# Kernel optimization log

Hardware: AMD Instinct MI355X
Metric: run time of the kernel (lower is better)

## Reference

```python
import jax, jax.numpy as jnp
import numpy as np

N = 50000      # nodes
E = 500000     # edges
F = 128        # hidden_dim
NRBF = 20
CUTOFF = 5.0


def setup_inputs() -> dict:
    key = jax.random.key(0)
    ks = jax.random.split(key, 12)
    s = jax.random.normal(ks[0], (N, F), dtype=jnp.float32)
    v = jax.random.normal(ks[1], (N, 3, F), dtype=jnp.float32)
    pos = jax.random.normal(ks[2], (N, 3), dtype=jnp.float32)
    src = jax.random.randint(ks[3], (E,), 0, N)
    # avoid self-loops so rij never degenerates to exactly zero
    off = jax.random.randint(ks[4], (E,), 1, N)
    dst = (src + off) % N
    edge_index = jnp.stack([src, dst]).astype(jnp.int64)
    in_dim = 2 * F + NRBF
    sc = 0.02
    W1 = jax.random.normal(ks[5], (in_dim, 2 * F), dtype=jnp.float32) * sc
    b1 = jnp.zeros((2 * F,), dtype=jnp.float32)
    W2 = jax.random.normal(ks[6], (2 * F, 2 * F), dtype=jnp.float32) * sc
    b2 = jnp.zeros((2 * F,), dtype=jnp.float32)
    Ws = jax.random.normal(ks[7], (2 * F, F), dtype=jnp.float32) * sc
    bs = jnp.zeros((F,), dtype=jnp.float32)
    Wv = jax.random.normal(ks[8], (2 * F, F), dtype=jnp.float32) * sc
    bv = jnp.zeros((F,), dtype=jnp.float32)
    centers = jnp.linspace(0.0, CUTOFF, NRBF).astype(jnp.float32)
    delta = centers[1] - centers[0]
    widths = jnp.full((NRBF,), delta, dtype=jnp.float32)
    return {"s": s, "v": v, "pos": pos, "edge_index": edge_index,
            "W1": W1, "b1": b1, "W2": W2, "b2": b2,
            "Ws": Ws, "bs": bs, "Wv": Wv, "bv": bv,
            "centers": centers, "widths": widths}


def reference(s, v, pos, edge_index, W1, b1, W2, b2, Ws, bs, Wv, bv, centers, widths):
    src, dst = edge_index[0], edge_index[1]
    rij = pos[dst] - pos[src]                          # [E,3]
    dist = jnp.linalg.norm(rij, axis=-1, keepdims=True)  # [E,1]
    rbf = jnp.exp(-((dist - centers) / (widths + 1e-8)) ** 2)  # [E,NRBF]
    h = jnp.concatenate([s[src], s[dst], rbf], axis=-1)  # [E, 2F+NRBF]
    h = jax.nn.silu(h @ W1 + b1)
    h = jax.nn.silu(h @ W2 + b2)                         # [E, 2F]
    ds_edge = h @ Ws + bs                                # [E, F]
    dv_mag = h @ Wv + bv                                 # [E, F]
    safe = jnp.where(dist > 0, dist, 1.0)
    inv_dist = jnp.where(dist > 0, 1.0 / safe, 0.0)
    directions = rij * inv_dist                          # [E,3]
    dv_edge = directions[:, :, None] * dv_mag[:, None, :]  # [E,3,F]
    num_nodes = s.shape[0]
    ds = jax.ops.segment_sum(ds_edge, dst, num_segments=num_nodes)   # [N,F]
    dv = jax.ops.segment_sum(dv_edge, dst, num_segments=num_nodes)   # [N,3,F]
    return s + ds, v + dv
```

## Files before the change

kernel.cpp:

```cpp
#include <hip/hip_runtime.h>
#include <math.h>

#define FDIM   128
#define TWOF   256
#define NRBF_  20
#define INDIM  276
#define K1PAD  288
#define XS     296
#define HS     264
#define EOS    264
#define TE     64

typedef __bf16 bf16x8 __attribute__((ext_vector_type(8)));
typedef __bf16 bf16x4 __attribute__((ext_vector_type(4)));
typedef float  f32x4  __attribute__((ext_vector_type(4)));

__device__ inline float blo(unsigned p){ return __uint_as_float(p << 16); }
__device__ inline float bhi(unsigned p){ return __uint_as_float(p & 0xffff0000u); }


__global__ void sniff_idx(const int* __restrict__ ei, int nsample, int* __restrict__ flag) {
    __shared__ int any;
    if (threadIdx.x == 0) any = 0;
    __syncthreads();
    int nz = 0;
    for (int i = threadIdx.x; i < nsample; i += blockDim.x)
        nz |= (ei[2 * i + 1] != 0);
    if (nz) atomicOr(&any, 1);
    __syncthreads();
    if (threadIdx.x == 0) *flag = any;
}

__global__ void init_out(const float4* __restrict__ s4, const float4* __restrict__ v4,
                         float4* __restrict__ out4, int nf4, int total4) {
    for (int i = blockIdx.x * blockDim.x + threadIdx.x; i < total4;
         i += gridDim.x * blockDim.x)
        out4[i] = (i < nf4) ? s4[i] : v4[i - nf4];
}

__global__ void prep_weights(const float* __restrict__ W1, const float* __restrict__ W2,
                             const float* __restrict__ Ws, const float* __restrict__ Wv,
                             __bf16* __restrict__ W1t, __bf16* __restrict__ W2t,
                             __bf16* __restrict__ W3t) {
    int id = blockIdx.x * 256 + threadIdx.x;
    const int n1 = 256 * K1PAD;
    if (id < n1) {
        int n = id / K1PAD, k = id - n * K1PAD;
        W1t[id] = (k < INDIM) ? (__bf16)W1[k * TWOF + n] : (__bf16)0.f;
    } else if (id < n1 + 65536) {
        int j = id - n1; int n = j >> 8, k = j & 255;
        W2t[j] = (__bf16)W2[k * TWOF + n];
    } else if (id < n1 + 131072) {
        int j = id - n1 - 65536; int n = j >> 8, k = j & 255;
        W3t[j] = (n < FDIM) ? (__bf16)Ws[k * FDIM + n]
                            : (__bf16)Wv[k * FDIM + (n - FDIM)];
    }
}


__global__ void zero_hist(int* __restrict__ hist, int N) {
    int i = blockIdx.x * 256 + threadIdx.x;
    if (i < N) hist[i] = 0;
}

__global__ void hist_k(const int* __restrict__ ei, const int* __restrict__ flag,
                       int* __restrict__ hist, int E) {
    int e = blockIdx.x * 256 + threadIdx.x;
    if (e >= E) return;
    int dst = (*flag == 0) ? ei[2 * (E + e)] : ei[E + e];
    atomicAdd(&hist[dst], 1);
}

__global__ void scan_a(const int* __restrict__ hist, int* __restrict__ loc,
                       int* __restrict__ bsum, int N) {
    __shared__ int sums[256];
    int t = threadIdx.x;
    int base = blockIdx.x * 1024 + t * 4;
    int v0 = (base + 0 < N) ? hist[base + 0] : 0;
    int v1 = (base + 1 < N) ? hist[base + 1] : 0;
    int v2 = (base + 2 < N) ? hist[base + 2] : 0;
    int v3 = (base + 3 < N) ? hist[base + 3] : 0;
    int s = v0 + v1 + v2 + v3;
    sums[t] = s;
    __syncthreads();
    for (int off = 1; off < 256; off <<= 1) {
        int x = (t >= off) ? sums[t - off] : 0;
        __syncthreads();
        sums[t] += x;
        __syncthreads();
    }
    int excl = sums[t] - s;
    if (t == 255) bsum[blockIdx.x] = sums[255];
    if (base + 0 < N) loc[base + 0] = excl; excl += v0;
    if (base + 1 < N) loc[base + 1] = excl; excl += v1;
    if (base + 2 < N) loc[base + 2] = excl; excl += v2;
    if (base + 3 < N) loc[base + 3] = excl;
}

__global__ void scan_b(int* __restrict__ bsum, int nb) {
    if (threadIdx.x == 0 && blockIdx.x == 0) {
        int run = 0;
        for (int i = 0; i < nb; ++i) { int v = bsum[i]; bsum[i] = run; run += v; }
    }
}

__global__ void scan_c(const int* __restrict__ loc, const int* __restrict__ bsum,
                       int* __restrict__ rs, int* __restrict__ cursor, int N, int E) {
    int i = blockIdx.x * 256 + threadIdx.x;
    if (i < N) {
        int v = loc[i] + bsum[i >> 10];
        rs[i] = v; cursor[i] = v;
    }
    if (i == 0) rs[N] = E;
}

__global__ void scatter_k(const int* __restrict__ ei, const int* __restrict__ flag,
                          int* __restrict__ cursor, int* __restrict__ elist, int E) {
    int e = blockIdx.x * 256 + threadIdx.x;
    if (e >= E) return;
    int dst = (*flag == 0) ? ei[2 * (E + e)] : ei[E + e];
    int pos = atomicAdd(&cursor[dst], 1);
    elist[pos] = e;
}


template<int CSR>
__launch_bounds__(256, 2)
__global__ void edge_kernel(const float* __restrict__ s,
                            const float* __restrict__ pos,
                            const int* __restrict__ ei,
                            const float* __restrict__ b1, const float* __restrict__ b2,
                            const float* __restrict__ bsm, const float* __restrict__ bvm,
                            const float* __restrict__ centers, const float* __restrict__ widths,
                            const __bf16* __restrict__ W1t, const __bf16* __restrict__ W2t,
                            const __bf16* __restrict__ W3t,
                            const int* __restrict__ flag,
                            __bf16* __restrict__ EO,
                            float* __restrict__ dirx, float* __restrict__ diry,
                            float* __restrict__ dirz,
                            float* __restrict__ out, int N, int E) {
    __shared__ __align__(16) __bf16 Xs[TE][XS];
    __shared__ __align__(16) __bf16 Hs[TE][HS];
    __shared__ float sdir[3][TE];
    __shared__ int ssrc[TE], sdst[TE], svalid[TE];

    const int t    = threadIdx.x;
    const int lane = t & 63;
    const int wave = t >> 6;
    const int e0   = blockIdx.x * TE;
    const int i64  = (*flag == 0);

    if (t < TE) {
        int e = e0 + t;
        int valid = (e < E);
        int srcn = 0, dstn = 0;
        if (valid) {
            if (i64) { srcn = ei[2 * e]; dstn = ei[2 * (E + e)]; }
            else     { srcn = ei[e];     dstn = ei[E + e]; }
        }
        ssrc[t] = srcn; sdst[t] = dstn; svalid[t] = valid;
        float rx = pos[dstn * 3 + 0] - pos[srcn * 3 + 0];
        float ry = pos[dstn * 3 + 1] - pos[srcn * 3 + 1];
        float rz = pos[dstn * 3 + 2] - pos[srcn * 3 + 2];
        float dist = sqrtf(rx * rx + ry * ry + rz * rz);
        float inv = dist > 0.f ? 1.f / dist : 0.f;
        float dx = rx * inv, dy = ry * inv, dz = rz * inv;
        sdir[0][t] = dx; sdir[1][t] = dy; sdir[2][t] = dz;
        if (CSR && valid) { dirx[e] = dx; diry[e] = dy; dirz[e] = dz; }
#pragma unroll
        for (int k = 0; k < 32; ++k) {
            float val = 0.f;
            if (k < NRBF_) {
                float u = (dist - centers[k]) / (widths[k] + 1e-8f);
                val = __expf(-u * u);
            }
            Xs[t][TWOF + k] = (__bf16)val;
        }
    }
    __syncthreads();

    {
        const int half = lane >> 5;
        const int q    = lane & 31;
        const float4* s4 = (const float4*)s;
#pragma unroll 4
        for (int i = 0; i < 16; ++i) {
            int e = wave * 16 + i;
            int node = half ? sdst[e] : ssrc[e];
            float4 x = s4[node * 32 + q];
            bf16x4 b; b.x = (__bf16)x.x; b.y = (__bf16)x.y; b.z = (__bf16)x.z; b.w = (__bf16)x.w;
            *(bf16x4*)&Xs[e][half * FDIM + q * 4] = b;
        }
    }
    __syncthreads();

    const int l15 = lane & 15;
    const int kg  = (lane >> 4) * 8;
    const int nbase = wave * 64;

    f32x4 acc[4][4];

#pragma unroll
    for (int et = 0; et < 4; ++et)
#pragma unroll
        for (int nt = 0; nt < 4; ++nt) acc[et][nt] = (f32x4)0.f;
    {
        const __bf16* bp[4];
#pragma unroll
        for (int nt = 0; nt < 4; ++nt)
            bp[nt] = &W1t[(size_t)(nbase + nt * 16 + l15) * K1PAD + kg];
        bf16x8 bcur[4];
#pragma unroll
        for (int nt = 0; nt < 4; ++nt) bcur[nt] = *(const bf16x8*)bp[nt];
#pragma unroll
        for (int kc = 0; kc < K1PAD; kc += 32) {
            bf16x8 bnxt[4];
            if (kc + 32 < K1PAD) {
#pragma unroll
                for (int nt = 0; nt < 4; ++nt)
                    bnxt[nt] = *(const bf16x8*)(bp[nt] + kc + 32);
            }
            bf16x8 a[4];
#pragma unroll
            for (int et = 0; et < 4; ++et)
                a[et] = *(const bf16x8*)&Xs[et * 16 + l15][kc + kg];
#pragma unroll
            for (int nt = 0; nt < 4; ++nt)
#pragma unroll
                for (int et = 0; et < 4; ++et)
                    acc[et][nt] = __builtin_amdgcn_mfma_f32_16x16x32_bf16(a[et], bcur[nt], acc[et][nt], 0, 0, 0);
#pragma unroll
            for (int nt = 0; nt < 4; ++nt) bcur[nt] = bnxt[nt];
        }
    }
#pragma unroll
    for (int nt = 0; nt < 4; ++nt) {
        int n = nbase + nt * 16 + l15;
        float bb = b1[n];
#pragma unroll
        for (int et = 0; et < 4; ++et)
#pragma unroll
            for (int r = 0; r < 4; ++r) {
                int m = et * 16 + (lane >> 4) * 4 + r;
                float h = acc[et][nt][r] + bb;
                Hs[m][n] = (__bf16)(h * __builtin_amdgcn_rcpf(1.f + __expf(-h)));
            }
    }
    __syncthreads();

#pragma unroll
    for (int et = 0; et < 4; ++et)
#pragma unroll
        for (int nt = 0; nt < 4; ++nt) acc[et][nt] = (f32x4)0.f;
    {
        const __bf16* bp[4];
#pragma unroll
        for (int nt = 0; nt < 4; ++nt)
            bp[nt] = &W2t[(size_t)(nbase + nt * 16 + l15) * TWOF + kg];
        bf16x8 bcur[4];
#pragma unroll
        for (int nt = 0; nt < 4; ++nt) bcur[nt] = *(const bf16x8*)bp[nt];
#pragma unroll
        for (int kc = 0; kc < TWOF; kc += 32) {
            bf16x8 bnxt[4];
            if (kc + 32 < TWOF) {
#pragma unroll
                for (int nt = 0; nt < 4; ++nt)
                    bnxt[nt] = *(const bf16x8*)(bp[nt] + kc + 32);
            }
            bf16x8 a[4];
#pragma unroll
            for (int et = 0; et < 4; ++et)
                a[et] = *(const bf16x8*)&Hs[et * 16 + l15][kc + kg];
#pragma unroll
            for (int nt = 0; nt < 4; ++nt)
#pragma unroll
                for (int et = 0; et < 4; ++et)
                    acc[et][nt] = __builtin_amdgcn_mfma_f32_16x16x32_bf16(a[et], bcur[nt], acc[et][nt], 0, 0, 0);
#pragma unroll
            for (int nt = 0; nt < 4; ++nt) bcur[nt] = bnxt[nt];
        }
    }
    __syncthreads();
#pragma unroll
    for (int nt = 0; nt < 4; ++nt) {
        int n = nbase + nt * 16 + l15;
        float bb = b2[n];
#pragma unroll
        for (int et = 0; et < 4; ++et)
#pragma unroll
            for (int r = 0; r < 4; ++r) {
                int m = et * 16 + (lane >> 4) * 4 + r;
                float h = acc[et][nt][r] + bb;
                Hs[m][n] = (__bf16)(h * __builtin_amdgcn_rcpf(1.f + __expf(-h)));
            }
    }
    __syncthreads();

#pragma unroll
    for (int et = 0; et < 4; ++et)
#pragma unroll
        for (int nt = 0; nt < 4; ++nt) acc[et][nt] = (f32x4)0.f;
    {
        const __bf16* bp[4];
#pragma unroll
        for (int nt = 0; nt < 4; ++nt) {
            int rowbase = ((nt >= 2) ? FDIM : 0) + wave * 32 + (nt & 1) * 16 + l15;
            bp[nt] = &W3t[(size_t)rowbase * TWOF + kg];
        }
        bf16x8 bcur[4];
#pragma unroll
        for (int nt = 0; nt < 4; ++nt) bcur[nt] = *(const bf16x8*)bp[nt];
#pragma unroll
        for (int kc = 0; kc < TWOF; kc += 32) {
            bf16x8 bnxt[4];
            if (kc + 32 < TWOF) {
#pragma unroll
                for (int nt = 0; nt < 4; ++nt)
                    bnxt[nt] = *(const bf16x8*)(bp[nt] + kc + 32);
            }
            bf16x8 a[4];
#pragma unroll
            for (int et = 0; et < 4; ++et)
                a[et] = *(const bf16x8*)&Hs[et * 16 + l15][kc + kg];
#pragma unroll
            for (int nt = 0; nt < 4; ++nt)
#pragma unroll
                for (int et = 0; et < 4; ++et)
                    acc[et][nt] = __builtin_amdgcn_mfma_f32_16x16x32_bf16(a[et], bcur[nt], acc[et][nt], 0, 0, 0);
#pragma unroll
            for (int nt = 0; nt < 4; ++nt) bcur[nt] = bnxt[nt];
        }
    }

    float b3v[4];
#pragma unroll
    for (int nt = 0; nt < 4; ++nt) {
        int n = wave * 32 + (nt & 1) * 16 + l15;
        b3v[nt] = (nt < 2) ? bsm[n] : bvm[n];
    }

    if (CSR) {
        __bf16 (*EOs)[EOS] = (__bf16(*)[EOS])(&Xs[0][0]);
#pragma unroll
        for (int nt = 0; nt < 4; ++nt) {
            int col = ((nt >= 2) ? FDIM : 0) + wave * 32 + (nt & 1) * 16 + l15;
            float bb = b3v[nt];
#pragma unroll
            for (int et = 0; et < 4; ++et)
#pragma unroll
                for (int r = 0; r < 4; ++r) {
                    int m = et * 16 + (lane >> 4) * 4 + r;
                    EOs[m][col] = (__bf16)(acc[et][nt][r] + bb);
                }
        }
        __syncthreads();
        uint4* dst4 = (uint4*)(EO + (size_t)e0 * 256);
#pragma unroll
        for (int j = 0; j < 8; ++j) {
            int flat = j * 256 + t;
            int row = flat >> 5, col = flat & 31;
            dst4[(size_t)row * 32 + col] = *(const uint4*)&EOs[row][col * 8];
        }
    } else {
        float* outs = out;
        float* outv = out + (size_t)N * FDIM;
#pragma unroll
        for (int et = 0; et < 4; ++et) {
#pragma unroll
            for (int r = 0; r < 4; ++r) {
                int m = et * 16 + (lane >> 4) * 4 + r;
                if (!svalid[m]) continue;
                int dst = sdst[m];
                float dx = sdir[0][m], dy = sdir[1][m], dz = sdir[2][m];
#pragma unroll
                for (int nt = 0; nt < 4; ++nt) {
                    int n = wave * 32 + (nt & 1) * 16 + l15;
                    float val = acc[et][nt][r] + b3v[nt];
                    if (nt < 2) {
                        atomicAdd(&outs[dst * FDIM + n], val);
                    } else {
                        int base = dst * 3 * FDIM + n;
                        atomicAdd(&outv[base],            dx * val);
                        atomicAdd(&outv[base + FDIM],     dy * val);
                        atomicAdd(&outv[base + 2 * FDIM], dz * val);
                    }
                }
            }
        }
    }
}


__launch_bounds__(256)
__global__ void node_kernel(const float* __restrict__ s, const float* __restrict__ v,
                            const __bf16* __restrict__ EO,
                            const float* __restrict__ dirx, const float* __restrict__ diry,
                            const float* __restrict__ dirz,
                            const int* __restrict__ rs, const int* __restrict__ elist,
                            float* __restrict__ out, int N) {
    int wave = threadIdx.x >> 6, lane = threadIdx.x & 63;
    int n = blockIdx.x * 4 + wave;
    if (n >= N) return;
    int beg = rs[n], end = rs[n + 1];

    float a0 = 0.f, a1 = 0.f;
    float vx0 = 0.f, vx1 = 0.f, vy0 = 0.f, vy1 = 0.f, vz0 = 0.f, vz1 = 0.f;
    const unsigned* EO32 = (const unsigned*)EO;

    for (int i = beg; i < end; ++i) {
        int e = elist[i];
        unsigned pds = EO32[(size_t)e * 128 + lane];
        unsigned pvm = EO32[(size_t)e * 128 + 64 + lane];
        float dx = dirx[e], dy = diry[e], dz = dirz[e];
        float d0 = blo(pds), d1 = bhi(pds);
        float m0 = blo(pvm), m1 = bhi(pvm);
        a0 += d0; a1 += d1;
        vx0 = fmaf(dx, m0, vx0); vx1 = fmaf(dx, m1, vx1);
        vy0 = fmaf(dy, m0, vy0); vy1 = fmaf(dy, m1, vy1);
        vz0 = fmaf(dz, m0, vz0); vz1 = fmaf(dz, m1, vz1);
    }

    float2 sv = ((const float2*)&s[(size_t)n * FDIM])[lane];
    float2 o0 = { sv.x + a0, sv.y + a1 };
    ((float2*)&out[(size_t)n * FDIM])[lane] = o0;

    const float* vb = &v[(size_t)n * 3 * FDIM];
    float* ovb = &out[(size_t)N * FDIM + (size_t)n * 3 * FDIM];
    float2 vv;
    vv = ((const float2*)vb)[lane];
    ((float2*)ovb)[lane] = { vv.x + vx0, vv.y + vx1 };
    vv = ((const float2*)(vb + FDIM))[lane];
    ((float2*)(ovb + FDIM))[lane] = { vv.x + vy0, vv.y + vy1 };
    vv = ((const float2*)(vb + 2 * FDIM))[lane];
    ((float2*)(ovb + 2 * FDIM))[lane] = { vv.x + vz0, vv.y + vz1 };
}


static inline size_t align256(size_t x) { return (x + 255) & ~(size_t)255; }

extern "C" void kernel_launch(void* const* d_in, const int* in_sizes, int n_in,
                              void* d_out, int out_size, void* d_ws, size_t ws_size,
                              hipStream_t stream) {
    const float* s   = (const float*)d_in[0];
    const float* v   = (const float*)d_in[1];
    const float* pos = (const float*)d_in[2];
    const int*   ei  = (const int*)d_in[3];
    const float* W1  = (const float*)d_in[4];
    const float* b1  = (const float*)d_in[5];
    const float* W2  = (const float*)d_in[6];
    const float* b2  = (const float*)d_in[7];
    const float* Wsm = (const float*)d_in[8];
    const float* bsm = (const float*)d_in[9];
    const float* Wvm = (const float*)d_in[10];
    const float* bvm = (const float*)d_in[11];
    const float* centers = (const float*)d_in[12];
    const float* widths  = (const float*)d_in[13];
    float* out = (float*)d_out;

    int N = in_sizes[0] / FDIM;
    int E = in_sizes[3] / 2;
    int nblocks = (E + TE - 1) / TE;

    size_t off = 0;
    int* flag = (int*)((char*)d_ws + off);           off = align256(off + 4);
    __bf16* W1t = (__bf16*)((char*)d_ws + off);      off = align256(off + (size_t)256 * K1PAD * 2);
    __bf16* W2t = (__bf16*)((char*)d_ws + off);      off = align256(off + (size_t)256 * TWOF * 2);
    __bf16* W3t = (__bf16*)((char*)d_ws + off);      off = align256(off + (size_t)256 * TWOF * 2);
    int* hist   = (int*)((char*)d_ws + off);         off = align256(off + (size_t)N * 4);
    int* loc    = (int*)((char*)d_ws + off);         off = align256(off + (size_t)N * 4);
    int* bsum   = (int*)((char*)d_ws + off);         off = align256(off + 1024);
    int* rs     = (int*)((char*)d_ws + off);         off = align256(off + (size_t)(N + 1) * 4);
    int* cursor = (int*)((char*)d_ws + off);         off = align256(off + (size_t)N * 4);
    int* elist  = (int*)((char*)d_ws + off);         off = align256(off + (size_t)E * 4);
    float* dirx = (float*)((char*)d_ws + off);       off = align256(off + (size_t)E * 4);
    float* diry = (float*)((char*)d_ws + off);       off = align256(off + (size_t)E * 4);
    float* dirz = (float*)((char*)d_ws + off);       off = align256(off + (size_t)E * 4);
    __bf16* EO  = (__bf16*)((char*)d_ws + off);      off = align256(off + (size_t)nblocks * TE * 256 * 2);
    bool use_csr = (off <= ws_size);

    int nsample = E < 1024 ? E : 1024;
    hipLaunchKernelGGL(sniff_idx, dim3(1), dim3(256), 0, stream, ei, nsample, flag);

    int nprep = 256 * K1PAD + 2 * 256 * TWOF;
    hipLaunchKernelGGL(prep_weights, dim3((nprep + 255) / 256), dim3(256), 0, stream,
                       W1, W2, Wsm, Wvm, W1t, W2t, W3t);

    if (use_csr) {
        int nb = (N + 1023) / 1024;
        hipLaunchKernelGGL(zero_hist, dim3((N + 255) / 256), dim3(256), 0, stream, hist, N);
        hipLaunchKernelGGL(hist_k, dim3((E + 255) / 256), dim3(256), 0, stream, ei, flag, hist, E);
        hipLaunchKernelGGL(scan_a, dim3(nb), dim3(256), 0, stream, hist, loc, bsum, N);
        hipLaunchKernelGGL(scan_b, dim3(1), dim3(64), 0, stream, bsum, nb);
        hipLaunchKernelGGL(scan_c, dim3((N + 255) / 256), dim3(256), 0, stream, loc, bsum, rs, cursor, N, E);
        hipLaunchKernelGGL(scatter_k, dim3((E + 255) / 256), dim3(256), 0, stream, ei, flag, cursor, elist, E);

        hipLaunchKernelGGL(edge_kernel<1>, dim3(nblocks), dim3(256), 0, stream,
                           s, pos, ei, b1, b2, bsm, bvm, centers, widths,
                           W1t, W2t, W3t, flag, EO, dirx, diry, dirz, out, N, E);

        hipLaunchKernelGGL(node_kernel, dim3((N + 3) / 4), dim3(256), 0, stream,
                           s, v, EO, dirx, diry, dirz, rs, elist, out, N);
    } else {
        int nf4    = (N * FDIM) / 4;
        int total4 = N * FDIM;
        hipLaunchKernelGGL(init_out, dim3(8192), dim3(256), 0, stream,
                           (const float4*)s, (const float4*)v, (float4*)out, nf4, total4);
        hipLaunchKernelGGL(edge_kernel<0>, dim3(nblocks), dim3(256), 0, stream,
                           s, pos, ei, b1, b2, bsm, bvm, centers, widths,
                           W1t, W2t, W3t, flag, EO, dirx, diry, dirz, out, N, E);
    }
}
```

Measured before the change: 806.6 us.

## Write edge outputs in dst-sorted order and merge LDS buffers for occupancy

Result: faster. 776.5 us (-3.7%).

```diff
diff --git a/kernel.cpp b/kernel.cpp
--- a/kernel.cpp
+++ b/kernel.cpp
@@ -7,8 +7,6 @@
 #define INDIM  276
 #define K1PAD  288
 #define XS     296
-#define HS     264
-#define EOS    264
 #define TE     64
 
 typedef __bf16 bf16x8 __attribute__((ext_vector_type(8)));
@@ -115,17 +113,17 @@
 }
 
 __global__ void scatter_k(const int* __restrict__ ei, const int* __restrict__ flag,
-                          int* __restrict__ cursor, int* __restrict__ elist, int E) {
+                          int* __restrict__ cursor, int* __restrict__ perm, int E) {
     int e = blockIdx.x * 256 + threadIdx.x;
     if (e >= E) return;
     int dst = (*flag == 0) ? ei[2 * (E + e)] : ei[E + e];
     int pos = atomicAdd(&cursor[dst], 1);
-    elist[pos] = e;
+    perm[e] = pos;
 }
 
 
 template<int CSR>
-__launch_bounds__(256, 2)
+__launch_bounds__(256, 4)
 __global__ void edge_kernel(const float* __restrict__ s,
                             const float* __restrict__ pos,
                             const int* __restrict__ ei,
@@ -135,14 +133,14 @@
                             const __bf16* __restrict__ W1t, const __bf16* __restrict__ W2t,
                             const __bf16* __restrict__ W3t,
                             const int* __restrict__ flag,
+                            const int* __restrict__ perm,
                             __bf16* __restrict__ EO,
                             float* __restrict__ dirx, float* __restrict__ diry,
                             float* __restrict__ dirz,
                             float* __restrict__ out, int N, int E) {
-    __shared__ __align__(16) __bf16 Xs[TE][XS];
-    __shared__ __align__(16) __bf16 Hs[TE][HS];
+    __shared__ __align__(16) __bf16 Sb[TE][XS];
     __shared__ float sdir[3][TE];
-    __shared__ int ssrc[TE], sdst[TE], svalid[TE];
+    __shared__ int ssrc[TE], sdst[TE], svalid[TE], sperm[TE];
 
     const int t    = threadIdx.x;
     const int lane = t & 63;
@@ -166,7 +164,12 @@
         float inv = dist > 0.f ? 1.f / dist : 0.f;
         float dx = rx * inv, dy = ry * inv, dz = rz * inv;
         sdir[0][t] = dx; sdir[1][t] = dy; sdir[2][t] = dz;
-        if (CSR && valid) { dirx[e] = dx; diry[e] = dy; dirz[e] = dz; }
+        int p = 0;
+        if (CSR && valid) {
+            p = perm[e];
+            dirx[p] = dx; diry[p] = dy; dirz[p] = dz;
+        }
+        sperm[t] = p;
 #pragma unroll
         for (int k = 0; k < 32; ++k) {
             float val = 0.f;
@@ -174,7 +177,7 @@
                 float u = (dist - centers[k]) / (widths[k] + 1e-8f);
                 val = __expf(-u * u);
             }
-            Xs[t][TWOF + k] = (__bf16)val;
+            Sb[t][TWOF + k] = (__bf16)val;
         }
     }
     __syncthreads();
@@ -189,7 +192,7 @@
             int node = half ? sdst[e] : ssrc[e];
             float4 x = s4[node * 32 + q];
             bf16x4 b; b.x = (__bf16)x.x; b.y = (__bf16)x.y; b.z = (__bf16)x.z; b.w = (__bf16)x.w;
-            *(bf16x4*)&Xs[e][half * FDIM + q * 4] = b;
+            *(bf16x4*)&Sb[e][half * FDIM + q * 4] = b;
         }
     }
     __syncthreads();
@@ -223,7 +226,7 @@
             bf16x8 a[4];
 #pragma unroll
             for (int et = 0; et < 4; ++et)
-                a[et] = *(const bf16x8*)&Xs[et * 16 + l15][kc + kg];
+                a[et] = *(const bf16x8*)&Sb[et * 16 + l15][kc + kg];
 #pragma unroll
             for (int nt = 0; nt < 4; ++nt)
 #pragma unroll
@@ -233,6 +236,7 @@
             for (int nt = 0; nt < 4; ++nt) bcur[nt] = bnxt[nt];
         }
     }
+    __syncthreads();
 #pragma unroll
     for (int nt = 0; nt < 4; ++nt) {
         int n = nbase + nt * 16 + l15;
@@ -243,7 +247,7 @@
             for (int r = 0; r < 4; ++r) {
                 int m = et * 16 + (lane >> 4) * 4 + r;
                 float h = acc[et][nt][r] + bb;
-                Hs[m][n] = (__bf16)(h * __builtin_amdgcn_rcpf(1.f + __expf(-h)));
+                Sb[m][n] = (__bf16)(h * __builtin_amdgcn_rcpf(1.f + __expf(-h)));
             }
     }
     __syncthreads();
@@ -271,7 +275,7 @@
             bf16x8 a[4];
 #pragma unroll
             for (int et = 0; et < 4; ++et)
-                a[et] = *(const bf16x8*)&Hs[et * 16 + l15][kc + kg];
+                a[et] = *(const bf16x8*)&Sb[et * 16 + l15][kc + kg];
 #pragma unroll
             for (int nt = 0; nt < 4; ++nt)
 #pragma unroll
@@ -292,7 +296,7 @@
             for (int r = 0; r < 4; ++r) {
                 int m = et * 16 + (lane >> 4) * 4 + r;
                 float h = acc[et][nt][r] + bb;
-                Hs[m][n] = (__bf16)(h * __builtin_amdgcn_rcpf(1.f + __expf(-h)));
+                Sb[m][n] = (__bf16)(h * __builtin_amdgcn_rcpf(1.f + __expf(-h)));
             }
     }
     __syncthreads();
@@ -322,7 +326,7 @@
             bf16x8 a[4];
 #pragma unroll
             for (int et = 0; et < 4; ++et)
-                a[et] = *(const bf16x8*)&Hs[et * 16 + l15][kc + kg];
+                a[et] = *(const bf16x8*)&Sb[et * 16 + l15][kc + kg];
 #pragma unroll
             for (int nt = 0; nt < 4; ++nt)
 #pragma unroll
@@ -341,7 +345,8 @@
     }
 
     if (CSR) {
-        __bf16 (*EOs)[EOS] = (__bf16(*)[EOS])(&Xs[0][0]);
+        __syncthreads();
+        __bf16 (*EOs)[XS] = (__bf16(*)[XS])(&Sb[0][0]);
 #pragma unroll
         for (int nt = 0; nt < 4; ++nt) {
             int col = ((nt >= 2) ? FDIM : 0) + wave * 32 + (nt & 1) * 16 + l15;
@@ -355,12 +360,13 @@
                 }
         }
         __syncthreads();
-        uint4* dst4 = (uint4*)(EO + (size_t)e0 * 256);
+        uint4* dst4 = (uint4*)EO;
 #pragma unroll
         for (int j = 0; j < 8; ++j) {
             int flat = j * 256 + t;
             int row = flat >> 5, col = flat & 31;
-            dst4[(size_t)row * 32 + col] = *(const uint4*)&EOs[row][col * 8];
+            if (!svalid[row]) continue;
+            dst4[(size_t)sperm[row] * 32 + col] = *(const uint4*)&EOs[row][col * 8];
         }
     } else {
         float* outs = out;
@@ -397,7 +403,7 @@
                             const __bf16* __restrict__ EO,
                             const float* __restrict__ dirx, const float* __restrict__ diry,
                             const float* __restrict__ dirz,
-                            const int* __restrict__ rs, const int* __restrict__ elist,
+                            const int* __restrict__ rs,
                             float* __restrict__ out, int N) {
     int wave = threadIdx.x >> 6, lane = threadIdx.x & 63;
     int n = blockIdx.x * 4 + wave;
@@ -408,11 +414,11 @@
     float vx0 = 0.f, vx1 = 0.f, vy0 = 0.f, vy1 = 0.f, vz0 = 0.f, vz1 = 0.f;
     const unsigned* EO32 = (const unsigned*)EO;
 
+#pragma unroll 2
     for (int i = beg; i < end; ++i) {
-        int e = elist[i];
-        unsigned pds = EO32[(size_t)e * 128 + lane];
-        unsigned pvm = EO32[(size_t)e * 128 + 64 + lane];
-        float dx = dirx[e], dy = diry[e], dz = dirz[e];
+        unsigned pds = EO32[(size_t)i * 128 + lane];
+        unsigned pvm = EO32[(size_t)i * 128 + 64 + lane];
+        float dx = dirx[i], dy = diry[i], dz = dirz[i];
         float d0 = blo(pds), d1 = bhi(pds);
         float m0 = blo(pvm), m1 = bhi(pvm);
         a0 += d0; a1 += d1;
@@ -422,8 +428,7 @@
     }
 
     float2 sv = ((const float2*)&s[(size_t)n * FDIM])[lane];
-    float2 o0 = { sv.x + a0, sv.y + a1 };
-    ((float2*)&out[(size_t)n * FDIM])[lane] = o0;
+    ((float2*)&out[(size_t)n * FDIM])[lane] = { sv.x + a0, sv.y + a1 };
 
     const float* vb = &v[(size_t)n * 3 * FDIM];
     float* ovb = &out[(size_t)N * FDIM + (size_t)n * 3 * FDIM];
@@ -472,11 +477,11 @@
     int* bsum   = (int*)((char*)d_ws + off);         off = align256(off + 1024);
     int* rs     = (int*)((char*)d_ws + off);         off = align256(off + (size_t)(N + 1) * 4);
     int* cursor = (int*)((char*)d_ws + off);         off = align256(off + (size_t)N * 4);
-    int* elist  = (int*)((char*)d_ws + off);         off = align256(off + (size_t)E * 4);
+    int* perm   = (int*)((char*)d_ws + off);         off = align256(off + (size_t)E * 4);
     float* dirx = (float*)((char*)d_ws + off);       off = align256(off + (size_t)E * 4);
     float* diry = (float*)((char*)d_ws + off);       off = align256(off + (size_t)E * 4);
     float* dirz = (float*)((char*)d_ws + off);       off = align256(off + (size_t)E * 4);
-    __bf16* EO  = (__bf16*)((char*)d_ws + off);      off = align256(off + (size_t)nblocks * TE * 256 * 2);
+    __bf16* EO  = (__bf16*)((char*)d_ws + off);      off = align256(off + (size_t)E * 256 * 2);
     bool use_csr = (off <= ws_size);
 
     int nsample = E < 1024 ? E : 1024;
@@ -493,14 +498,14 @@
         hipLaunchKernelGGL(scan_a, dim3(nb), dim3(256), 0, stream, hist, loc, bsum, N);
         hipLaunchKernelGGL(scan_b, dim3(1), dim3(64), 0, stream, bsum, nb);
         hipLaunchKernelGGL(scan_c, dim3((N + 255) / 256), dim3(256), 0, stream, loc, bsum, rs, cursor, N, E);
-        hipLaunchKernelGGL(scatter_k, dim3((E + 255) / 256), dim3(256), 0, stream, ei, flag, cursor, elist, E);
+        hipLaunchKernelGGL(scatter_k, dim3((E + 255) / 256), dim3(256), 0, stream, ei, flag, cursor, perm, E);
 
         hipLaunchKernelGGL(edge_kernel<1>, dim3(nblocks), dim3(256), 0, stream,
                            s, pos, ei, b1, b2, bsm, bvm, centers, widths,
-                           W1t, W2t, W3t, flag, EO, dirx, diry, dirz, out, N, E);
+                           W1t, W2t, W3t, flag, perm, EO, dirx, diry, dirz, out, N, E);
 
         hipLaunchKernelGGL(node_kernel, dim3((N + 3) / 4), dim3(256), 0, stream,
-                           s, v, EO, dirx, diry, dirz, rs, elist, out, N);
+                           s, v, EO, dirx, diry, dirz, rs, out, N);
     } else {
         int nf4    = (N * FDIM) / 4;
         int total4 = N * FDIM;
@@ -508,6 +513,6 @@
                            (const float4*)s, (const float4*)v, (float4*)out, nf4, total4);
         hipLaunchKernelGGL(edge_kernel<0>, dim3(nblocks), dim3(256), 0, stream,
                            s, pos, ei, b1, b2, bsm, bvm, centers, widths,
-                           W1t, W2t, W3t, flag, EO, dirx, diry, dirz, out, N, E);
-    }
-}
+                           W1t, W2t, W3t, flag, perm, EO, dirx, diry, dirz, out, N, E);
+    }
+}
```
